# Performance work log

Hardware: AMD Instinct MI355X
Metric: run time of the kernel (lower is better)

## Reference

```python
import jax, jax.numpy as jnp
import numpy as np
from jax import lax

B, T, C = 4, 2048, 2048
H, S = 32, 64
HEAD_SIZE_DIVISOR = 8.0
LN_EPS = 1e-5


def setup_inputs() -> dict:
    key = jax.random.key(0)
    ks = jax.random.split(key, 12)
    scale = 0.02
    return {
        "hidden": jax.random.normal(ks[0], (B, T, C), jnp.float32),
        "state_kv": jnp.zeros((B, H, S, S), jnp.float32),
        "time_decay": jax.random.normal(ks[1], (H, S), jnp.float32) * 0.5,
        "time_faaaa": jax.random.normal(ks[2], (H, S), jnp.float32) * 0.5,
        "time_mix_key": jax.random.uniform(ks[3], (1, 1, C), jnp.float32),
        "time_mix_value": jax.random.uniform(ks[4], (1, 1, C), jnp.float32),
        "time_mix_receptance": jax.random.uniform(ks[5], (1, 1, C), jnp.float32),
        "time_mix_gate": jax.random.uniform(ks[6], (1, 1, C), jnp.float32),
        "key_w": jax.random.normal(ks[7], (C, C), jnp.float32) * scale,
        "value_w": jax.random.normal(ks[8], (C, C), jnp.float32) * scale,
        "receptance_w": jax.random.normal(ks[9], (C, C), jnp.float32) * scale,
        "gate_w": jax.random.normal(ks[10], (C, C), jnp.float32) * scale,
        "output_w": jax.random.normal(ks[11], (C, C), jnp.float32) * scale,
        "ln_w": jnp.ones((C,), jnp.float32),
        "ln_b": jnp.zeros((C,), jnp.float32),
    }


def _rwkv5_scan(r, k, v, w, u, state0):
    # r,k,v: [B,T,H,S]; w,u: [H,S]; state0: [B,H,S,S]
    w_ = w[None, :, :, None]  # decay broadcast over value dim
    u_ = u[None, :, :, None]  # time_first (bonus) broadcast over value dim

    def step(state, rkv):
        rt, kt, vt = rkv  # each [B,H,S]
        a = kt[:, :, :, None] * vt[:, :, None, :]      # outer product [B,H,S,S]
        o = jnp.einsum("bhs,bhsd->bhd", rt, u_ * a + state)
        state = a + w_ * state
        return state, o

    rt = jnp.moveaxis(r, 1, 0)  # [T,B,H,S]
    kt = jnp.moveaxis(k, 1, 0)
    vt = jnp.moveaxis(v, 1, 0)
    state_f, out = lax.scan(step, state0, (rt, kt, vt))
    return jnp.moveaxis(out, 0, 1), state_f  # [B,T,H,S], [B,H,S,S]


def reference(hidden, state_kv, time_decay, time_faaaa, time_mix_key,
              time_mix_value, time_mix_receptance, time_mix_gate,
              key_w, value_w, receptance_w, gate_w, output_w, ln_w, ln_b):
    B_, T_, C_ = hidden.shape
    H_, S_ = time_faaaa.shape

    # time shift: prepend zero row, drop last (state=None path)
    shifted = jnp.pad(hidden, ((0, 0), (1, 0), (0, 0)))[:, :-1]

    mix = lambda m: hidden * m + shifted * (1.0 - m)
    k = mix(time_mix_key) @ key_w.T
    v = mix(time_mix_value) @ value_w.T
    r = mix(time_mix_receptance) @ receptance_w.T
    gate = jax.nn.silu(mix(time_mix_gate) @ gate_w.T)

    r = r.reshape(B_, T_, H_, S_)
    k = k.reshape(B_, T_, H_, S_)
    v = v.reshape(B_, T_, H_, S_)

    w = jnp.exp(-jnp.exp(time_decay))  # [H,S]
    out, state_f = _rwkv5_scan(r, k, v, w, time_faaaa, state_kv)

    # GroupNorm over H groups of size S, applied per (b,t) row
    x = out.reshape(B_ * T_, H_, S_) / HEAD_SIZE_DIVISOR
    mu = jnp.mean(x, axis=-1, keepdims=True)
    var = jnp.var(x, axis=-1, keepdims=True)
    xn = (x - mu) * lax.rsqrt(var + LN_EPS)
    xn = xn.reshape(B_ * T_, H_ * S_) * ln_w + ln_b

    out = xn.reshape(B_, T_, C_) * gate
    out = out @ output_w.T
    return out, state_f
```

## Files before the change

kernel.cpp:

```cpp
#include <hip/hip_runtime.h>
#include <hip/hip_bf16.h>

typedef unsigned short u16;
typedef __bf16 bf16x8 __attribute__((ext_vector_type(8)));
typedef unsigned short ushort8v __attribute__((ext_vector_type(8)));
typedef float f32x4 __attribute__((ext_vector_type(4)));
typedef float f32x8 __attribute__((ext_vector_type(8)));

#define B_ 4
#define T_ 2048
#define C_ 2048
#define H_ 32
#define S_ 64

__device__ __forceinline__ u16 f2bf(float x) {
  unsigned int u = __float_as_uint(x);
  unsigned int r = (u + 0x7fffu + ((u >> 16) & 1u)) >> 16;
  return (u16)r;
}
__device__ __forceinline__ float bf2f(u16 x) {
  return __uint_as_float(((unsigned int)x) << 16);
}
__device__ __forceinline__ void gload_lds16(const void* g, void* l) {
  __builtin_amdgcn_global_load_lds(
      (const __attribute__((address_space(1))) void*)g,
      (__attribute__((address_space(3))) void*)l, 16, 0, 0);
}

#define VM10 asm volatile("s_waitcnt vmcnt(10)" ::: "memory")
#define VM8 asm volatile("s_waitcnt vmcnt(8)" ::: "memory")
#define VM4 asm volatile("s_waitcnt vmcnt(4)" ::: "memory")
#define VM0 asm volatile("s_waitcnt vmcnt(0)" ::: "memory")
#define BARR __builtin_amdgcn_s_barrier()
#define SCB __builtin_amdgcn_sched_barrier(0)

__global__ __launch_bounds__(256) void mix_cast_kernel(
    const float* __restrict__ hidden, const float* __restrict__ mixp,
    u16* __restrict__ out) {
  int idx = blockIdx.x * 256 + threadIdx.x;
  int c4 = idx & 511;
  int bt = idx >> 9;
  int t = bt & (T_ - 1);
  float4 h = reinterpret_cast<const float4*>(hidden)[idx];
  float4 m = reinterpret_cast<const float4*>(mixp)[c4];
  float4 sh = make_float4(0.f, 0.f, 0.f, 0.f);
  if (t != 0) sh = reinterpret_cast<const float4*>(hidden)[idx - 512];
  ushort4 o;
  o.x = f2bf(h.x * m.x + sh.x * (1.f - m.x));
  o.y = f2bf(h.y * m.y + sh.y * (1.f - m.y));
  o.z = f2bf(h.z * m.z + sh.z * (1.f - m.z));
  o.w = f2bf(h.w * m.w + sh.w * (1.f - m.w));
  reinterpret_cast<ushort4*>(out)[idx] = o;
}

__global__ __launch_bounds__(256) void mix4_cast_kernel(
    const float* __restrict__ hidden,
    const float* __restrict__ mK, const float* __restrict__ mV,
    const float* __restrict__ mR, const float* __restrict__ mG,
    u16* __restrict__ oK, u16* __restrict__ oV,
    u16* __restrict__ oR, u16* __restrict__ oG) {
  int idx = blockIdx.x * 256 + threadIdx.x;
  int c4 = idx & 511;
  int bt = idx >> 9;
  int t = bt & (T_ - 1);
  float4 h = reinterpret_cast<const float4*>(hidden)[idx];
  float4 sh = make_float4(0.f, 0.f, 0.f, 0.f);
  if (t != 0) sh = reinterpret_cast<const float4*>(hidden)[idx - 512];
  float4 m;
  ushort4 o;
#define DOMIX(MP, OP)                                          \
  m = reinterpret_cast<const float4*>(MP)[c4];                 \
  o.x = f2bf(h.x * m.x + sh.x * (1.f - m.x));                  \
  o.y = f2bf(h.y * m.y + sh.y * (1.f - m.y));                  \
  o.z = f2bf(h.z * m.z + sh.z * (1.f - m.z));                  \
  o.w = f2bf(h.w * m.w + sh.w * (1.f - m.w));                  \
  reinterpret_cast<ushort4*>(OP)[idx] = o;
  DOMIX(mK, oK)
  DOMIX(mV, oV)
  DOMIX(mR, oR)
  DOMIX(mG, oG)
#undef DOMIX
}

__global__ __launch_bounds__(256) void conv_bf16_kernel(
    const float* __restrict__ in, u16* __restrict__ out, int n4) {
  int i = blockIdx.x * 256 + threadIdx.x;
  if (i >= n4) return;
  float4 v = reinterpret_cast<const float4*>(in)[i];
  ushort4 o;
  o.x = f2bf(v.x); o.y = f2bf(v.y); o.z = f2bf(v.z); o.w = f2bf(v.w);
  reinterpret_cast<ushort4*>(out)[i] = o;
}

template <typename OT>
__global__ __launch_bounds__(512, 2) void gemm_bt256(
    const u16* __restrict__ A, const u16* __restrict__ Bm,
    OT* __restrict__ C, int M, int N, int K) {
  __shared__ u16 Asl[4][8192];
  __shared__ u16 Bsl[4][8192];
  const int tid = threadIdx.x, lane = tid & 63, w = tid >> 6;
  const int wr = w >> 2, wc = w & 3;
  const int nbn = N >> 8;
  const int nwg = gridDim.x, bid = blockIdx.x, cpx = nwg >> 3;
  const int swz = (bid & 7) * cpx + (bid >> 3);
  const int bm = swz / nbn, bn = swz % nbn;
  const int Ar0 = bm * 256, Br0 = bn * 256;

  const int rowoff = w * 32 + (lane >> 2);
  const int colswz = ((lane & 3) ^ ((lane >> 3) & 3)) * 8;
  const u16* Agl = A + (size_t)(Ar0 + rowoff) * K + colswz;
  const u16* Bgl = Bm + (size_t)(Br0 + rowoff) * K + colswz;
  const int lb = w * 1024;

  const int rdc = (((lane >> 4) ^ ((lane >> 1) & 3))) * 8;
  const int arow = wr * 128 + (lane & 15);
  const int brow = wc * 64 + (lane & 15);

  f32x4 acc[8][4];
#pragma unroll
  for (int m = 0; m < 8; m++)
#pragma unroll
    for (int n = 0; n < 4; n++) acc[m][n] = (f32x4){0.f, 0.f, 0.f, 0.f};

  auto STA = [&](int ktile, int kk, int slot) {
    const u16* g = Agl + ktile * 64 + kk * 32;
    gload_lds16(g, &Asl[slot][lb]);
    gload_lds16(g + (size_t)16 * K, &Asl[slot][lb + 512]);
  };
  auto STB = [&](int ktile, int kk, int slot) {
    const u16* g = Bgl + ktile * 64 + kk * 32;
    gload_lds16(g, &Bsl[slot][lb]);
    gload_lds16(g + (size_t)16 * K, &Bsl[slot][lb + 512]);
  };
  auto PH = [&](int P, int kk, int mh) {
    const u16* As_ = Asl[P * 2 + kk];
    const u16* Bs_ = Bsl[P * 2 + kk];
    bf16x8 af[4], bv[4];
    int ab = (arow + mh * 64) * 32 + rdc;
#pragma unroll
    for (int mf = 0; mf < 4; mf++)
      af[mf] = __builtin_bit_cast(bf16x8, *reinterpret_cast<const ushort8v*>(&As_[ab + mf * 512]));
    int bb = brow * 32 + rdc;
#pragma unroll
    for (int nf = 0; nf < 4; nf++)
      bv[nf] = __builtin_bit_cast(bf16x8, *reinterpret_cast<const ushort8v*>(&Bs_[bb + nf * 512]));
    __builtin_amdgcn_s_setprio(1);
#pragma unroll
    for (int mf = 0; mf < 4; mf++)
#pragma unroll
      for (int nf = 0; nf < 4; nf++)
        acc[mh * 4 + mf][nf] =
            __builtin_amdgcn_mfma_f32_16x16x32_bf16(af[mf], bv[nf], acc[mh * 4 + mf][nf], 0, 0, 0);
    __builtin_amdgcn_s_setprio(0);
  };

  const int NT = K >> 6;
  STA(0, 0, 0); STB(0, 0, 0);
  STA(0, 1, 1); STB(0, 1, 1);
  STA(1, 0, 2); STB(1, 0, 2);

  for (int T = 0; T + 2 < NT; ++T) {
    int P = T & 1, Q = P ^ 1;
    STA(T + 1, 1, Q * 2 + 1); STB(T + 1, 1, Q * 2 + 1);
    VM10; BARR; SCB; PH(P, 0, 0); PH(P, 0, 1); BARR;
    STA(T + 2, 0, P * 2 + 0); STB(T + 2, 0, P * 2 + 0);
    VM10; BARR; SCB; PH(P, 1, 0); PH(P, 1, 1); BARR;
  }
  {
    int T = NT - 2, P = T & 1, Q = P ^ 1;
    STA(T + 1, 1, Q * 2 + 1); STB(T + 1, 1, Q * 2 + 1);
    VM10; BARR; SCB; PH(P, 0, 0); PH(P, 0, 1); BARR;
    VM8; BARR; SCB; PH(P, 1, 0); PH(P, 1, 1); BARR;
  }
  {
    int P = (NT - 1) & 1;
    VM4; BARR; SCB; PH(P, 0, 0); PH(P, 0, 1); BARR;
    VM0; BARR; SCB; PH(P, 1, 0); PH(P, 1, 1);
  }

  int crow0 = Ar0 + wr * 128 + (lane >> 4) * 4;
  int ccol0 = Br0 + wc * 64 + (lane & 15);
#pragma unroll
  for (int mfg = 0; mfg < 8; mfg++) {
#pragma unroll
    for (int q = 0; q < 4; q++) {
      OT* cp = C + (size_t)(crow0 + mfg * 16 + q) * N + ccol0;
#pragma unroll
      for (int nf = 0; nf < 4; nf++) {
        if constexpr (sizeof(OT) == 2)
          cp[nf * 16] = (OT)f2bf(acc[mfg][nf][q]);
        else
          cp[nf * 16] = (OT)acc[mfg][nf][q];
      }
    }
  }
}

template <int CHL>
__global__ __launch_bounds__(64) void scan_phase1_mfma(
    const u16* __restrict__ Kb, const u16* __restrict__ Vb,
    const float* __restrict__ td, float* __restrict__ chunks) {
  constexpr int NCH = T_ / CHL;
  constexpr int LDW = CHL + 8;
  __shared__ u16 Ash[64 * LDW];
  __shared__ u16 Vsh[64 * LDW];
  int lane = threadIdx.x & 63;
  int gw = blockIdx.x;
  int c = gw & (NCH - 1), bh = gw / NCH;
  int h = bh & 31, b = bh >> 5;

  size_t base = ((size_t)b * T_ + (size_t)c * CHL) * C_ + h * 64 + lane;
  const u16* Kp = Kb + base;
  const u16* Vp = Vb + base;

  {
    float w = __expf(-__expf(td[h * 64 + lane]));
    u16* Arow = &Ash[lane * LDW];
    float p = 1.f;
#pragma unroll
    for (int i4 = CHL - 4; i4 >= 0; i4 -= 4) {
      float a3 = bf2f(Kp[(size_t)(i4 + 3) * C_]) * p; p *= w;
      float a2 = bf2f(Kp[(size_t)(i4 + 2) * C_]) * p; p *= w;
      float a1 = bf2f(Kp[(size_t)(i4 + 1) * C_]) * p; p *= w;
      float a0 = bf2f(Kp[(size_t)(i4 + 0) * C_]) * p; p *= w;
      ushort4 pk;
      pk.x = f2bf(a0); pk.y = f2bf(a1); pk.z = f2bf(a2); pk.w = f2bf(a3);
      *reinterpret_cast<ushort4*>(&Arow[i4]) = pk;
    }
  }
  {
    u16* Vrow = &Vsh[lane * LDW];
#pragma unroll
    for (int i4 = 0; i4 < CHL; i4 += 4) {
      ushort4 pk;
      pk.x = Vp[(size_t)(i4 + 0) * C_];
      pk.y = Vp[(size_t)(i4 + 1) * C_];
      pk.z = Vp[(size_t)(i4 + 2) * C_];
      pk.w = Vp[(size_t)(i4 + 3) * C_];
      *reinterpret_cast<ushort4*>(&Vrow[i4]) = pk;
    }
  }

  f32x4 acc[4][4];
#pragma unroll
  for (int m = 0; m < 4; m++)
#pragma unroll
    for (int n = 0; n < 4; n++) acc[m][n] = (f32x4){0.f, 0.f, 0.f, 0.f};

#pragma unroll
  for (int kb = 0; kb < CHL / 32; kb++) {
    int ko = kb * 32 + (lane >> 4) * 8;
    bf16x8 Af[4], Bf[4];
#pragma unroll
    for (int m = 0; m < 4; m++) {
      ushort8v t8 = *reinterpret_cast<const ushort8v*>(&Ash[(m * 16 + (lane & 15)) * LDW + ko]);
      Af[m] = __builtin_bit_cast(bf16x8, t8);
    }
#pragma unroll
    for (int n = 0; n < 4; n++) {
      ushort8v t8 = *reinterpret_cast<const ushort8v*>(&Vsh[(n * 16 + (lane & 15)) * LDW + ko]);
      Bf[n] = __builtin_bit_cast(bf16x8, t8);
    }
#pragma unroll
    for (int m = 0; m < 4; m++)
#pragma unroll
      for (int n = 0; n < 4; n++)
        acc[m][n] = __builtin_amdgcn_mfma_f32_16x16x32_bf16(Af[m], Bf[n], acc[m][n], 0, 0, 0);
  }

  float* outp = chunks + (((size_t)c * B_ + b) * H_ + h) * 4096;
  int r0 = (lane >> 4) * 4, c0 = lane & 15;
#pragma unroll
  for (int m = 0; m < 4; m++)
#pragma unroll
    for (int n = 0; n < 4; n++)
#pragma unroll
      for (int q = 0; q < 4; q++)
        outp[(size_t)(m * 16 + r0 + q) * 64 + n * 16 + c0] = acc[m][n][q];
}

template <int NCH, int CHL>
__global__ __launch_bounds__(256) void scan_phase1(
    const u16* __restrict__ Kb, const u16* __restrict__ Vb,
    const float* __restrict__ td, float* __restrict__ chunks) {
  int lane = threadIdx.x & 63;
  int gw = (blockIdx.x * 256 + threadIdx.x) >> 6;
  int c = gw & (NCH - 1), bh = gw / NCH;
  int h = bh & 31, b = bh >> 5;
  const float* tdh = td + h * 64;
  float wreg[64];
#pragma unroll
  for (int s = 0; s < 64; s++) wreg[s] = __expf(-__expf(tdh[s]));
  float st[64];
#pragma unroll
  for (int s = 0; s < 64; s++) st[s] = 0.f;
  size_t base = ((size_t)b * T_ + (size_t)c * CHL) * C_ + h * 64 + lane;
  const u16* Kp = Kb + base;
  const u16* Vp = Vb + base;
  for (int t = 0; t < CHL; t++) {
    float kcur = bf2f(Kp[(size_t)t * C_]), vcur = bf2f(Vp[(size_t)t * C_]);
#pragma unroll
    for (int s = 0; s < 64; s++) {
      float ks = __shfl(kcur, s);
      st[s] = fmaf(wreg[s], st[s], ks * vcur);
    }
  }
  float* outp = chunks + (((size_t)c * B_ + b) * H_ + h) * 4096 + lane;
#pragma unroll
  for (int s = 0; s < 64; s++) outp[s * 64] = st[s];
}

template <int NCH, int CHL>
__global__ __launch_bounds__(256) void scan_phase2(
    const float* __restrict__ st0, const float* __restrict__ td,
    float* __restrict__ chunks, float* __restrict__ state_out) {
  int idx = blockIdx.x * 256 + threadIdx.x;
  int h = (idx >> 12) & 31;
  int s = (idx >> 6) & 63;
  float wL = __expf(-(float)CHL * __expf(td[h * 64 + s]));
  float st = st0[idx];
#pragma unroll
  for (int cc = 0; cc < NCH; cc++) {
    size_t off = (size_t)cc * 524288 + idx;
    float sc = chunks[off];
    chunks[off] = st;
    st = fmaf(wL, st, sc);
  }
  state_out[idx] = st;
}

__global__ __launch_bounds__(64) void scan_phase3_mfma(
    const u16* __restrict__ Rb, const u16* __restrict__ Kb,
    const u16* __restrict__ Vb, const float* __restrict__ td,
    const float* __restrict__ tf, const float* __restrict__ chunks,
    const u16* __restrict__ Gb, const float* __restrict__ lnw,
    const float* __restrict__ lnb, u16* __restrict__ Y) {
  __shared__ __align__(16) u16 smem[5248];
  int lane = threadIdx.x & 63;
  int gw = blockIdx.x;
  int c = gw & 31, bh = gw >> 5;
  int h = bh & 31, b = bh >> 5;
  int a = lane & 15, g = lane >> 4;
  int h0 = h * 64;

  u16* Kt = smem;
  u16* Vt = Kt + 1024;
  u16* StT = Vt + 1024;
  u16* AT = StT + 2560;

  f32x8 sA[2], sB[2], sC[2];
#pragma unroll
  for (int kk = 0; kk < 2; kk++) {
#pragma unroll
    for (int e = 0; e < 8; e++) {
      int s = kk * 32 + g * 8 + e;
      float ew = __expf(td[h0 + s]);
      sA[kk][e] = __expf(-(float)a * ew);
      sB[kk][e] = __expf(-((float)a - 8.f) * ew);
      sC[kk][e] = __expf(-(7.f - (float)a) * ew);
    }
  }
  f32x4 sE[4];
  f32x4 ewD;
#pragma unroll
  for (int ms = 0; ms < 4; ms++) {
    ewD[ms] = __expf(td[h0 + ms * 16 + a]);
#pragma unroll
    for (int q = 0; q < 4; q++)
      sE[ms][q] = __expf(-16.f * __expf(td[h0 + ms * 16 + g * 4 + q]));
  }

  f32x4 St[4][4];
  const float* cpc = chunks + (((size_t)c * B_ + b) * H_ + h) * 4096;
#pragma unroll
  for (int ms = 0; ms < 4; ms++)
#pragma unroll
    for (int nd = 0; nd < 4; nd++)
#pragma unroll
      for (int q = 0; q < 4; q++)
        St[ms][nd][q] = cpc[(size_t)(ms * 16 + g * 4 + q) * 64 + nd * 16 + a];

#pragma unroll
  for (int z = 0; z < 6; z++) {
    int idx = z * 64 + lane;
    int row = idx / 24, col = 16 + idx % 24;
    AT[row * 40 + col] = 0;
  }

  size_t tbase = ((size_t)b * T_ + (size_t)c * 64) * C_ + h0;

  for (int sb = 0; sb < 4; sb++) {
    size_t rb0 = tbase + (size_t)(sb * 16) * C_;

    ushort8v r8[2], k8[2];
#pragma unroll
    for (int kk = 0; kk < 2; kk++) {
      r8[kk] = *reinterpret_cast<const ushort8v*>(Rb + rb0 + (size_t)a * C_ + kk * 32 + g * 8);
      k8[kk] = *reinterpret_cast<const ushort8v*>(Kb + rb0 + (size_t)a * C_ + kk * 32 + g * 8);
    }
    {
      int srow = lane >> 3;
      int scol = (lane & 7) * 8;
      *reinterpret_cast<ushort8v*>(&Kt[srow * 64 + scol]) =
          *reinterpret_cast<const ushort8v*>(Kb + rb0 + (size_t)srow * C_ + scol);
      *reinterpret_cast<ushort8v*>(&Kt[(srow + 8) * 64 + scol]) =
          *reinterpret_cast<const ushort8v*>(Kb + rb0 + (size_t)(srow + 8) * C_ + scol);
      *reinterpret_cast<ushort8v*>(&Vt[srow * 64 + scol]) =
          *reinterpret_cast<const ushort8v*>(Vb + rb0 + (size_t)srow * C_ + scol);
      *reinterpret_cast<ushort8v*>(&Vt[(srow + 8) * 64 + scol]) =
          *reinterpret_cast<const ushort8v*>(Vb + rb0 + (size_t)(srow + 8) * C_ + scol);
    }

    f32x4 O[4];
#pragma unroll
    for (int nd = 0; nd < 4; nd++) O[nd] = (f32x4){0.f, 0.f, 0.f, 0.f};

#pragma unroll
    for (int kk = 0; kk < 2; kk++) {
#pragma unroll
      for (int msl = 0; msl < 2; msl++) {
        int ms = kk * 2 + msl;
#pragma unroll
        for (int nd = 0; nd < 4; nd++) {
          ushort4 pk;
          pk.x = f2bf(St[ms][nd][0]); pk.y = f2bf(St[ms][nd][1]);
          pk.z = f2bf(St[ms][nd][2]); pk.w = f2bf(St[ms][nd][3]);
          *reinterpret_cast<ushort4*>(&StT[(a + nd * 16) * 40 + msl * 16 + g * 4]) = pk;
        }
      }
      ushort8v rt;
#pragma unroll
      for (int e = 0; e < 8; e++) rt[e] = f2bf(bf2f(r8[kk][e]) * sA[kk][e]);
      bf16x8 rtf = __builtin_bit_cast(bf16x8, rt);
#pragma unroll
      for (int nd = 0; nd < 4; nd++) {
        ushort8v sfr = *reinterpret_cast<const ushort8v*>(&StT[(a + nd * 16) * 40 + g * 8]);
        O[nd] = __builtin_amdgcn_mfma_f32_16x16x32_bf16(
            rtf, __builtin_bit_cast(bf16x8, sfr), O[nd], 0, 0, 0);
      }
    }

    float p = 0.f;
    {
      uintptr_t ta = (uintptr_t)(tf + h0);
      asm volatile("" : "+v"(ta));
      const float* tfp = (const float*)ta;
#pragma unroll
      for (int kk = 0; kk < 2; kk++) {
        float4 t0 = *reinterpret_cast<const float4*>(tfp + kk * 32 + g * 8);
        float4 t1 = *reinterpret_cast<const float4*>(tfp + kk * 32 + g * 8 + 4);
        float tv[8] = {t0.x, t0.y, t0.z, t0.w, t1.x, t1.y, t1.z, t1.w};
#pragma unroll
        for (int e = 0; e < 8; e++)
          p = fmaf(bf2f(r8[kk][e]) * tv[e], bf2f(k8[kk][e]), p);
      }
    }
    p += __shfl_xor(p, 16);
    p += __shfl_xor(p, 32);

    f32x4 Am = (f32x4){0.f, 0.f, 0.f, 0.f};
#pragma unroll
    for (int kk = 0; kk < 2; kk++) {
      ushort8v kh, rh;
#pragma unroll
      for (int e = 0; e < 8; e++) {
        kh[e] = f2bf(bf2f(k8[kk][e]) * sC[kk][e]);
        rh[e] = f2bf(bf2f(r8[kk][e]) * sB[kk][e]);
      }
      Am = __builtin_amdgcn_mfma_f32_16x16x32_bf16(
          __builtin_bit_cast(bf16x8, kh), __builtin_bit_cast(bf16x8, rh), Am, 0, 0, 0);
    }
    {
      ushort4 aw;
#pragma unroll
      for (int q = 0; q < 4; q++) {
        int jr = g * 4 + q;
        float v = (jr < a) ? Am[q] : ((jr == a) ? p : 0.f);
        ((u16*)&aw)[q] = f2bf(v);
      }
      *reinterpret_cast<ushort4*>(&AT[a * 40 + g * 4]) = aw;
    }
    bf16x8 afrag;
    {
      ushort8v t8 = *reinterpret_cast<const ushort8v*>(&AT[a * 40 + g * 8]);
      afrag = __builtin_bit_cast(bf16x8, t8);
    }

    bf16x8 vfrag[4];
#pragma unroll
    for (int nd = 0; nd < 4; nd++) {
      ushort8v t8;
      if (g < 2) {
#pragma unroll
        for (int e = 0; e < 8; e++) t8[e] = Vt[(g * 8 + e) * 64 + a + nd * 16];
      } else {
#pragma unroll
        for (int e = 0; e < 8; e++) t8[e] = 0;
      }
      vfrag[nd] = __builtin_bit_cast(bf16x8, t8);
    }

#pragma unroll
    for (int nd = 0; nd < 4; nd++)
      O[nd] = __builtin_amdgcn_mfma_f32_16x16x32_bf16(afrag, vfrag[nd], O[nd], 0, 0, 0);

#pragma unroll
    for (int ms = 0; ms < 4; ms++)
#pragma unroll
      for (int nd = 0; nd < 4; nd++)
#pragma unroll
        for (int q = 0; q < 4; q++) St[ms][nd][q] *= sE[ms][q];

#pragma unroll
    for (int ms = 0; ms < 4; ms++) {
      ushort8v kt8;
      if (g < 2) {
#pragma unroll
        for (int e = 0; e < 8; e++) {
          int j = g * 8 + e;
          float f = bf2f(Kt[j * 64 + ms * 16 + a]) * __expf(-(15.f - (float)j) * ewD[ms]);
          kt8[e] = f2bf(f);
        }
      } else {
#pragma unroll
        for (int e = 0; e < 8; e++) kt8[e] = 0;
      }
      bf16x8 kf = __builtin_bit_cast(bf16x8, kt8);
#pragma unroll
      for (int nd = 0; nd < 4; nd++)
        St[ms][nd] = __builtin_amdgcn_mfma_f32_16x16x32_bf16(kf, vfrag[nd], St[ms][nd], 0, 0, 0);
    }

#pragma unroll
    for (int nd = 0; nd < 4; nd++)
#pragma unroll
      for (int q = 0; q < 4; q++) O[nd][q] *= 0.125f;
    {
      uintptr_t la = (uintptr_t)(lnw + h0);
      uintptr_t lba = (uintptr_t)(lnb + h0);
      asm volatile("" : "+v"(la), "+v"(lba));
      const float* lwp = (const float*)la;
      const float* lbp = (const float*)lba;
#pragma unroll
      for (int q = 0; q < 4; q++) {
        float ssum = O[0][q] + O[1][q] + O[2][q] + O[3][q];
        ssum += __shfl_xor(ssum, 1); ssum += __shfl_xor(ssum, 2);
        ssum += __shfl_xor(ssum, 4); ssum += __shfl_xor(ssum, 8);
        float mean = ssum * (1.f / 64.f);
        float vv = 0.f;
#pragma unroll
        for (int nd = 0; nd < 4; nd++) {
          float d = O[nd][q] - mean;
          vv = fmaf(d, d, vv);
        }
        vv += __shfl_xor(vv, 1); vv += __shfl_xor(vv, 2);
        vv += __shfl_xor(vv, 4); vv += __shfl_xor(vv, 8);
        float rs = rsqrtf(vv * (1.f / 64.f) + 1e-5f);
        size_t rowoff = rb0 + (size_t)(g * 4 + q) * C_;
#pragma unroll
        for (int nd = 0; nd < 4; nd++) {
          float xn = (O[nd][q] - mean) * rs;
          float gv = bf2f(Gb[rowoff + nd * 16 + a]);
          float sg = gv / (1.f + __expf(-gv));
          Y[rowoff + nd * 16 + a] = f2bf((xn * lwp[nd * 16 + a] + lbp[nd * 16 + a]) * sg);
        }
      }
    }
  }
}

template <int NCH, int CHL>
__global__ __launch_bounds__(256) void scan_phase3(
    const u16* __restrict__ Rb, const u16* __restrict__ Kb,
    const u16* __restrict__ Vb, const float* __restrict__ td,
    const float* __restrict__ tf, const float* __restrict__ chunks,
    const u16* __restrict__ Gb, const float* __restrict__ lnw,
    const float* __restrict__ lnb, u16* __restrict__ Y) {
  int lane = threadIdx.x & 63;
  int gw = (blockIdx.x * 256 + threadIdx.x) >> 6;
  int c = gw & (NCH - 1), bh = gw / NCH;
  int h = bh & 31, b = bh >> 5;
  const float* tdh = td + h * 64;
  float wreg[64];
#pragma unroll
  for (int s = 0; s < 64; s++) wreg[s] = __expf(-__expf(tdh[s]));
  float u_own = tf[h * 64 + lane];
  float lw = lnw[h * 64 + lane];
  float lb = lnb[h * 64 + lane];
  float st[64];
  const float* cp = chunks + (((size_t)c * B_ + b) * H_ + h) * 4096 + lane;
#pragma unroll
  for (int s = 0; s < 64; s++) st[s] = cp[s * 64];
  size_t base = ((size_t)b * T_ + (size_t)c * CHL) * C_ + h * 64 + lane;
  const u16* Rp = Rb + base;
  const u16* Kp = Kb + base;
  const u16* Vp = Vb + base;
  const u16* Gp = Gb + base;
  u16* Yp = Y + base;
  for (int t = 0; t < CHL; t++) {
    float rcur = bf2f(Rp[(size_t)t * C_]);
    float kcur = bf2f(Kp[(size_t)t * C_]);
    float vcur = bf2f(Vp[(size_t)t * C_]);
    float p = rcur * u_own * kcur;
#pragma unroll
    for (int off = 32; off >= 1; off >>= 1) p += __shfl_xor(p, off);
    float acc = 0.f;
#pragma unroll
    for (int s = 0; s < 64; s++) {
      float rs = __shfl(rcur, s);
      float ks = __shfl(kcur, s);
      acc = fmaf(rs, st[s], acc);
      st[s] = fmaf(wreg[s], st[s], ks * vcur);
    }
    float o = fmaf(p, vcur, acc);
    float x = o * 0.125f;
    float sum = x;
#pragma unroll
    for (int off = 32; off >= 1; off >>= 1) sum += __shfl_xor(sum, off);
    float mean = sum * (1.f / 64.f);
    float d = x - mean;
    float v2 = d * d;
#pragma unroll
    for (int off = 32; off >= 1; off >>= 1) v2 += __shfl_xor(v2, off);
    float var = v2 * (1.f / 64.f);
    float xn = d * rsqrtf(var + 1e-5f);
    float gg = bf2f(Gp[(size_t)t * C_]);
    float sg = gg / (1.f + __expf(-gg));
    Yp[(size_t)t * C_] = f2bf((xn * lw + lb) * sg);
  }
}

extern "C" void kernel_launch(void* const* d_in, const int* in_sizes, int n_in,
                              void* d_out, int out_size, void* d_ws, size_t ws_size,
                              hipStream_t stream) {
  const float* hidden = (const float*)d_in[0];
  const float* state0 = (const float*)d_in[1];
  const float* td = (const float*)d_in[2];
  const float* tf = (const float*)d_in[3];
  const float* mk = (const float*)d_in[4];
  const float* mv = (const float*)d_in[5];
  const float* mr = (const float*)d_in[6];
  const float* mg = (const float*)d_in[7];
  const float* kw = (const float*)d_in[8];
  const float* vw = (const float*)d_in[9];
  const float* rw = (const float*)d_in[10];
  const float* gw = (const float*)d_in[11];
  const float* ow = (const float*)d_in[12];
  const float* lnw = (const float*)d_in[13];
  const float* lnb = (const float*)d_in[14];

  float* out = (float*)d_out;
  float* state_f = out + (size_t)B_ * T_ * C_;

  const size_t MBe = (size_t)B_ * T_ * C_;
  const size_t chunks32 = (size_t)32 * B_ * H_ * S_ * S_ * 4;

  size_t bigNeed = 4 * MBe * 2 + (size_t)C_ * C_ * 2 + 4 * MBe * 2 + chunks32;
  bool useBig = (ws_size >= bigNeed);

  dim3 blk(256);
  int mixGrid = (B_ * T_ * C_ / 4) / 256;
  int convN4 = C_ * C_ / 4;
  int convGrid = convN4 / 256;
  int gemmGrid = (B_ * T_ / 256) * (C_ / 256);
  dim3 gblk(512);

  if (useBig) {
    char* ws = (char*)d_ws;
    u16* mixR = (u16*)ws;  ws += MBe * 2;
    u16* mixK = (u16*)ws;  ws += MBe * 2;
    u16* mixV = (u16*)ws;  ws += MBe * 2;
    u16* mixG = (u16*)ws;  ws += MBe * 2;
    u16* wb = (u16*)ws;    ws += (size_t)C_ * C_ * 2;
    u16* rb = (u16*)ws;    ws += MBe * 2;
    u16* kb = (u16*)ws;    ws += MBe * 2;
    u16* vb = (u16*)ws;    ws += MBe * 2;
    u16* gb = (u16*)ws;    ws += MBe * 2;
    float* chunks = (float*)ws;

    mix4_cast_kernel<<<mixGrid, blk, 0, stream>>>(hidden, mk, mv, mr, mg,
                                                  mixK, mixV, mixR, mixG);
    conv_bf16_kernel<<<convGrid, blk, 0, stream>>>(rw, wb, convN4);
    gemm_bt256<u16><<<gemmGrid, gblk, 0, stream>>>(mixR, wb, rb, B_ * T_, C_, C_);
    conv_bf16_kernel<<<convGrid, blk, 0, stream>>>(kw, wb, convN4);
    gemm_bt256<u16><<<gemmGrid, gblk, 0, stream>>>(mixK, wb, kb, B_ * T_, C_, C_);
    conv_bf16_kernel<<<convGrid, blk, 0, stream>>>(vw, wb, convN4);
    gemm_bt256<u16><<<gemmGrid, gblk, 0, stream>>>(mixV, wb, vb, B_ * T_, C_, C_);
    conv_bf16_kernel<<<convGrid, blk, 0, stream>>>(gw, wb, convN4);
    gemm_bt256<u16><<<gemmGrid, gblk, 0, stream>>>(mixG, wb, gb, B_ * T_, C_, C_);

    scan_phase1_mfma<64><<<B_ * H_ * 32, dim3(64), 0, stream>>>(kb, vb, td, chunks);
    scan_phase2<32, 64><<<2048, blk, 0, stream>>>(state0, td, chunks, state_f);
    scan_phase3_mfma<<<B_ * H_ * 32, dim3(64), 0, stream>>>(rb, kb, vb, td, tf, chunks, gb, lnw, lnb, mixR);

    conv_bf16_kernel<<<convGrid, blk, 0, stream>>>(ow, wb, convN4);
    gemm_bt256<float><<<gemmGrid, gblk, 0, stream>>>(mixR, wb, out, B_ * T_, C_, C_);
    return;
  }

  char* ws = (char*)d_ws;
  u16* mixA = (u16*)ws;    ws += MBe * 2;
  u16* wb = (u16*)ws;      ws += (size_t)C_ * C_ * 2;
  u16* rb = (u16*)ws;      ws += MBe * 2;
  u16* kb = (u16*)ws;      ws += MBe * 2;
  u16* vb = (u16*)ws;      ws += MBe * 2;
  u16* gb = (u16*)ws;      ws += MBe * 2;
  float* chunks = (float*)ws;
  size_t fixed = (size_t)(ws - (char*)d_ws);
  bool use32 = (ws_size >= fixed + chunks32);

  mix_cast_kernel<<<mixGrid, blk, 0, stream>>>(hidden, mr, mixA);
  conv_bf16_kernel<<<convGrid, blk, 0, stream>>>(rw, wb, convN4);
  gemm_bt256<u16><<<gemmGrid, gblk, 0, stream>>>(mixA, wb, rb, B_ * T_, C_, C_);
  mix_cast_kernel<<<mixGrid, blk, 0, stream>>>(hidden, mk, mixA);
  conv_bf16_kernel<<<convGrid, blk, 0, stream>>>(kw, wb, convN4);
  gemm_bt256<u16><<<gemmGrid, gblk, 0, stream>>>(mixA, wb, kb, B_ * T_, C_, C_);
  mix_cast_kernel<<<mixGrid, blk, 0, stream>>>(hidden, mv, mixA);
  conv_bf16_kernel<<<convGrid, blk, 0, stream>>>(vw, wb, convN4);
  gemm_bt256<u16><<<gemmGrid, gblk, 0, stream>>>(mixA, wb, vb, B_ * T_, C_, C_);
  mix_cast_kernel<<<mixGrid, blk, 0, stream>>>(hidden, mg, mixA);
  conv_bf16_kernel<<<convGrid, blk, 0, stream>>>(gw, wb, convN4);
  gemm_bt256<u16><<<gemmGrid, gblk, 0, stream>>>(mixA, wb, gb, B_ * T_, C_, C_);

  if (use32) {
    scan_phase1_mfma<64><<<B_ * H_ * 32, dim3(64), 0, stream>>>(kb, vb, td, chunks);
    scan_phase2<32, 64><<<2048, blk, 0, stream>>>(state0, td, chunks, state_f);
    scan_phase3_mfma<<<B_ * H_ * 32, dim3(64), 0, stream>>>(rb, kb, vb, td, tf, chunks, gb, lnw, lnb, mixA);
  } else {
    scan_phase1<16, 128><<<(B_ * H_ * 16) / 4, blk, 0, stream>>>(kb, vb, td, chunks);
    scan_phase2<16, 128><<<2048, blk, 0, stream>>>(state0, td, chunks, state_f);
    scan_phase3<16, 128><<<(B_ * H_ * 16) / 4, blk, 0, stream>>>(rb, kb, vb, td, tf, chunks, gb, lnw, lnb, mixA);
  }

  conv_bf16_kernel<<<convGrid, blk, 0, stream>>>(ow, wb, convN4);
  gemm_bt256<float><<<gemmGrid, gblk, 0, stream>>>(mixA, wb, out, B_ * T_, C_, C_);
}
```

Measured before the change: 716.1 us.

## Restructure GEMM LDS staging to full-K-tile double buffer; prefetch scan subblocks

Result: slower. 787.5 us (+10.0%).

```diff
diff --git a/kernel.cpp b/kernel.cpp
--- a/kernel.cpp
+++ b/kernel.cpp
@@ -27,9 +27,7 @@
       (__attribute__((address_space(3))) void*)l, 16, 0, 0);
 }
 
-#define VM10 asm volatile("s_waitcnt vmcnt(10)" ::: "memory")
 #define VM8 asm volatile("s_waitcnt vmcnt(8)" ::: "memory")
-#define VM4 asm volatile("s_waitcnt vmcnt(4)" ::: "memory")
 #define VM0 asm volatile("s_waitcnt vmcnt(0)" ::: "memory")
 #define BARR __builtin_amdgcn_s_barrier()
 #define SCB __builtin_amdgcn_sched_barrier(0)
@@ -96,25 +94,23 @@
 __global__ __launch_bounds__(512, 2) void gemm_bt256(
     const u16* __restrict__ A, const u16* __restrict__ Bm,
     OT* __restrict__ C, int M, int N, int K) {
-  __shared__ u16 Asl[4][8192];
-  __shared__ u16 Bsl[4][8192];
+  __shared__ u16 Asl[2][2][8192];
+  __shared__ u16 Bsl[2][2][8192];
   const int tid = threadIdx.x, lane = tid & 63, w = tid >> 6;
   const int wr = w >> 2, wc = w & 3;
+  const int a15 = lane & 15, g4 = lane >> 4;
   const int nbn = N >> 8;
   const int nwg = gridDim.x, bid = blockIdx.x, cpx = nwg >> 3;
   const int swz = (bid & 7) * cpx + (bid >> 3);
   const int bm = swz / nbn, bn = swz % nbn;
   const int Ar0 = bm * 256, Br0 = bn * 256;
 
-  const int rowoff = w * 32 + (lane >> 2);
-  const int colswz = ((lane & 3) ^ ((lane >> 3) & 3)) * 8;
-  const u16* Agl = A + (size_t)(Ar0 + rowoff) * K + colswz;
-  const u16* Bgl = Bm + (size_t)(Br0 + rowoff) * K + colswz;
-  const int lb = w * 1024;
-
-  const int rdc = (((lane >> 4) ^ ((lane >> 1) & 3))) * 8;
-  const int arow = wr * 128 + (lane & 15);
-  const int brow = wc * 64 + (lane & 15);
+  const int strow = w * 16 + (lane >> 3);
+  const int sc0 = (((lane & 7) ^ ((lane >> 5) & 1)) * 8);
+  const int sc1 = sc0 ^ 16;
+  const u16* Abase = A + (size_t)(Ar0 + strow) * K;
+  const u16* Bbase = Bm + (size_t)(Br0 + strow) * K;
+  const int lwb = w * 1024;
 
   f32x4 acc[8][4];
 #pragma unroll
@@ -122,64 +118,63 @@
 #pragma unroll
     for (int n = 0; n < 4; n++) acc[m][n] = (f32x4){0.f, 0.f, 0.f, 0.f};
 
-  auto STA = [&](int ktile, int kk, int slot) {
-    const u16* g = Agl + ktile * 64 + kk * 32;
-    gload_lds16(g, &Asl[slot][lb]);
-    gload_lds16(g + (size_t)16 * K, &Asl[slot][lb + 512]);
+  auto STAGE = [&](int buf, int kt) {
+    const size_t ko = (size_t)kt * 64;
+#pragma unroll
+    for (int half = 0; half < 2; half++) {
+      const u16* ga = Abase + (size_t)half * 128 * K + ko;
+      const u16* gb = Bbase + (size_t)half * 128 * K + ko;
+      gload_lds16(ga + sc0, &Asl[buf][half][lwb]);
+      gload_lds16(ga + (size_t)8 * K + sc1, &Asl[buf][half][lwb + 512]);
+      gload_lds16(gb + sc0, &Bsl[buf][half][lwb]);
+      gload_lds16(gb + (size_t)8 * K + sc1, &Bsl[buf][half][lwb + 512]);
+    }
   };
-  auto STB = [&](int ktile, int kk, int slot) {
-    const u16* g = Bgl + ktile * 64 + kk * 32;
-    gload_lds16(g, &Bsl[slot][lb]);
-    gload_lds16(g + (size_t)16 * K, &Bsl[slot][lb + 512]);
-  };
-  auto PH = [&](int P, int kk, int mh) {
-    const u16* As_ = Asl[P * 2 + kk];
-    const u16* Bs_ = Bsl[P * 2 + kk];
+
+  const int rxor = (a15 >> 2) & 3;
+  auto PH = [&](int buf, int kk, int mg) {
+    const u16* Ah = Asl[buf][wr];
+    const u16* Bh = Bsl[buf][wc >> 1];
+    const int colr = kk * 32 + ((g4 ^ rxor) * 8);
     bf16x8 af[4], bv[4];
-    int ab = (arow + mh * 64) * 32 + rdc;
 #pragma unroll
     for (int mf = 0; mf < 4; mf++)
-      af[mf] = __builtin_bit_cast(bf16x8, *reinterpret_cast<const ushort8v*>(&As_[ab + mf * 512]));
-    int bb = brow * 32 + rdc;
+      af[mf] = __builtin_bit_cast(
+          bf16x8, *reinterpret_cast<const ushort8v*>(
+                      &Ah[((mg * 4 + mf) * 16 + a15) * 64 + colr]));
 #pragma unroll
     for (int nf = 0; nf < 4; nf++)
-      bv[nf] = __builtin_bit_cast(bf16x8, *reinterpret_cast<const ushort8v*>(&Bs_[bb + nf * 512]));
+      bv[nf] = __builtin_bit_cast(
+          bf16x8, *reinterpret_cast<const ushort8v*>(
+                      &Bh[((wc & 1) * 64 + nf * 16 + a15) * 64 + colr]));
     __builtin_amdgcn_s_setprio(1);
 #pragma unroll
     for (int mf = 0; mf < 4; mf++)
 #pragma unroll
       for (int nf = 0; nf < 4; nf++)
-        acc[mh * 4 + mf][nf] =
-            __builtin_amdgcn_mfma_f32_16x16x32_bf16(af[mf], bv[nf], acc[mh * 4 + mf][nf], 0, 0, 0);
+        acc[mg * 4 + mf][nf] = __builtin_amdgcn_mfma_f32_16x16x32_bf16(
+            af[mf], bv[nf], acc[mg * 4 + mf][nf], 0, 0, 0);
     __builtin_amdgcn_s_setprio(0);
   };
 
   const int NT = K >> 6;
-  STA(0, 0, 0); STB(0, 0, 0);
-  STA(0, 1, 1); STB(0, 1, 1);
-  STA(1, 0, 2); STB(1, 0, 2);
-
-  for (int T = 0; T + 2 < NT; ++T) {
-    int P = T & 1, Q = P ^ 1;
-    STA(T + 1, 1, Q * 2 + 1); STB(T + 1, 1, Q * 2 + 1);
-    VM10; BARR; SCB; PH(P, 0, 0); PH(P, 0, 1); BARR;
-    STA(T + 2, 0, P * 2 + 0); STB(T + 2, 0, P * 2 + 0);
-    VM10; BARR; SCB; PH(P, 1, 0); PH(P, 1, 1); BARR;
-  }
-  {
-    int T = NT - 2, P = T & 1, Q = P ^ 1;
-    STA(T + 1, 1, Q * 2 + 1); STB(T + 1, 1, Q * 2 + 1);
-    VM10; BARR; SCB; PH(P, 0, 0); PH(P, 0, 1); BARR;
-    VM8; BARR; SCB; PH(P, 1, 0); PH(P, 1, 1); BARR;
-  }
-  {
-    int P = (NT - 1) & 1;
-    VM4; BARR; SCB; PH(P, 0, 0); PH(P, 0, 1); BARR;
-    VM0; BARR; SCB; PH(P, 1, 0); PH(P, 1, 1);
-  }
-
-  int crow0 = Ar0 + wr * 128 + (lane >> 4) * 4;
-  int ccol0 = Br0 + wc * 64 + (lane & 15);
+  STAGE(0, 0);
+  for (int T = 0; T < NT; ++T) {
+    int buf = T & 1;
+    if (T + 1 < NT) {
+      STAGE(buf ^ 1, T + 1);
+      VM8;
+    } else {
+      VM0;
+    }
+    BARR; SCB;
+    PH(buf, 0, 0); PH(buf, 0, 1);
+    PH(buf, 1, 0); PH(buf, 1, 1);
+    BARR;
+  }
+
+  int crow0 = Ar0 + wr * 128 + g4 * 4;
+  int ccol0 = Br0 + wc * 64 + a15;
 #pragma unroll
   for (int mfg = 0; mfg < 8; mfg++) {
 #pragma unroll
@@ -388,28 +383,37 @@
   }
 
   size_t tbase = ((size_t)b * T_ + (size_t)c * 64) * C_ + h0;
-
+  int srow = lane >> 3;
+  int scol = (lane & 7) * 8;
+
+  ushort8v r8g[2][2], k8g[2][2], ksg[2][2], vsg[2][2];
+  auto LOADSB = [&](int s, int sbi) {
+    size_t rbx = tbase + (size_t)(sbi * 16) * C_;
+#pragma unroll
+    for (int kk = 0; kk < 2; kk++) {
+      r8g[s][kk] = *reinterpret_cast<const ushort8v*>(Rb + rbx + (size_t)a * C_ + kk * 32 + g * 8);
+      k8g[s][kk] = *reinterpret_cast<const ushort8v*>(Kb + rbx + (size_t)a * C_ + kk * 32 + g * 8);
+    }
+    ksg[s][0] = *reinterpret_cast<const ushort8v*>(Kb + rbx + (size_t)srow * C_ + scol);
+    ksg[s][1] = *reinterpret_cast<const ushort8v*>(Kb + rbx + (size_t)(srow + 8) * C_ + scol);
+    vsg[s][0] = *reinterpret_cast<const ushort8v*>(Vb + rbx + (size_t)srow * C_ + scol);
+    vsg[s][1] = *reinterpret_cast<const ushort8v*>(Vb + rbx + (size_t)(srow + 8) * C_ + scol);
+  };
+  LOADSB(0, 0);
+
+#pragma unroll
   for (int sb = 0; sb < 4; sb++) {
+    const int cu = sb & 1, nx = cu ^ 1;
     size_t rb0 = tbase + (size_t)(sb * 16) * C_;
 
-    ushort8v r8[2], k8[2];
-#pragma unroll
-    for (int kk = 0; kk < 2; kk++) {
-      r8[kk] = *reinterpret_cast<const ushort8v*>(Rb + rb0 + (size_t)a * C_ + kk * 32 + g * 8);
-      k8[kk] = *reinterpret_cast<const ushort8v*>(Kb + rb0 + (size_t)a * C_ + kk * 32 + g * 8);
-    }
-    {
-      int srow = lane >> 3;
-      int scol = (lane & 7) * 8;
-      *reinterpret_cast<ushort8v*>(&Kt[srow * 64 + scol]) =
-          *reinterpret_cast<const ushort8v*>(Kb + rb0 + (size_t)srow * C_ + scol);
-      *reinterpret_cast<ushort8v*>(&Kt[(srow + 8) * 64 + scol]) =
-          *reinterpret_cast<const ushort8v*>(Kb + rb0 + (size_t)(srow + 8) * C_ + scol);
-      *reinterpret_cast<ushort8v*>(&Vt[srow * 64 + scol]) =
-          *reinterpret_cast<const ushort8v*>(Vb + rb0 + (size_t)srow * C_ + scol);
-      *reinterpret_cast<ushort8v*>(&Vt[(srow + 8) * 64 + scol]) =
-          *reinterpret_cast<const ushort8v*>(Vb + rb0 + (size_t)(srow + 8) * C_ + scol);
-    }
+    *reinterpret_cast<ushort8v*>(&Kt[srow * 64 + scol]) = ksg[cu][0];
+    *reinterpret_cast<ushort8v*>(&Kt[(srow + 8) * 64 + scol]) = ksg[cu][1];
+    *reinterpret_cast<ushort8v*>(&Vt[srow * 64 + scol]) = vsg[cu][0];
+    *reinterpret_cast<ushort8v*>(&Vt[(srow + 8) * 64 + scol]) = vsg[cu][1];
+    ushort8v r8[2] = {r8g[cu][0], r8g[cu][1]};
+    ushort8v k8[2] = {k8g[cu][0], k8g[cu][1]};
+
+    if (sb < 3) LOADSB(nx, sb + 1);
 
     f32x4 O[4];
 #pragma unroll
```
